# Performance work log

Hardware: AMD Instinct MI355X
Metric: run time of the kernel (lower is better)

Reference implementation:

```python
import jax, jax.numpy as jnp
import numpy as np

B, T, C, H = 8, 4096, 1024, 128

def setup_inputs() -> dict:
    key = jax.random.key(0)
    k1, k2, k3, k4 = jax.random.split(key, 4)
    x = jax.random.normal(k1, (B, T, C), dtype=jnp.float32)
    # torch Linear default init scale ~ 1/sqrt(fan_in); use scaled normal
    s = 1.0 / np.sqrt(C)
    Wq = jax.random.normal(k2, (C, H), dtype=jnp.float32) * s
    Wk = jax.random.normal(k3, (C, H), dtype=jnp.float32) * s
    Wv = jax.random.normal(k4, (C, H), dtype=jnp.float32) * s
    return {"x": x, "Wq": Wq, "Wk": Wk, "Wv": Wv}

def reference(x, Wq, Wk, Wv):
    # q,k,v: [B,T,H]
    q = jnp.einsum('btc,ch->bth', x, Wq)
    k = jnp.einsum('btc,ch->bth', x, Wk)
    v = jnp.einsum('btc,ch->bth', x, Wv)
    scale = k.shape[-1] ** -0.5
    wei = jnp.einsum('bqh,bkh->bqk', q, k) * scale  # [B,T,T]
    causal = jnp.tril(jnp.ones((T, T), dtype=bool))
    wei = jnp.where(causal, wei, -jnp.inf)
    wei = jax.nn.softmax(wei, axis=-1)
    # dropout p=0.0 (eval): identity
    out = jnp.einsum('bqk,bkh->bqh', wei, v)  # [B,T,H]
    return out
```

## Files before the change

### kernel.cpp

```cpp
#include <hip/hip_runtime.h>

#define B_ 8
#define T_ 4096
#define C_ 1024
#define H_ 128

using bf16x8 = __attribute__((ext_vector_type(8))) __bf16;
using bf16x4 = __attribute__((ext_vector_type(4))) __bf16;
using f32x4  = __attribute__((ext_vector_type(4))) float;

__device__ __forceinline__ unsigned short f2bf(float f) {
    union { float f; unsigned u; } v; v.f = f;
    unsigned u = v.u;
    u += 0x7FFF + ((u >> 16) & 1);
    return (unsigned short)(u >> 16);
}
__device__ __forceinline__ ushort4 pack4(const f32x4 v) {
    ushort4 p; p.x = f2bf(v[0]); p.y = f2bf(v[1]); p.z = f2bf(v[2]); p.w = f2bf(v[3]);
    return p;
}
__device__ __forceinline__ ushort4 pack4f(const float4 v) {
    ushort4 p; p.x = f2bf(v.x); p.y = f2bf(v.y); p.z = f2bf(v.z); p.w = f2bf(v.w);
    return p;
}

__global__ __launch_bounds__(256) void wt_kernel(const float* __restrict__ Wq,
                                                 const float* __restrict__ Wk,
                                                 const float* __restrict__ Wv,
                                                 unsigned short* __restrict__ wt) {
    int idx = blockIdx.x * 256 + threadIdx.x;
    int w = idx / (C_ * H_);
    int r = idx - w * (C_ * H_);
    int c = r >> 7;
    int h = r & (H_ - 1);
    const float* W = (w == 0) ? Wq : (w == 1) ? Wk : Wv;
    wt[((size_t)w * H_ + h) * C_ + c] = f2bf(W[r]);
}

#define PLDA 40
__global__ __launch_bounds__(256, 4) void proj_kernel(
        const float* __restrict__ x, const unsigned short* __restrict__ wt,
        unsigned short* __restrict__ q, unsigned short* __restrict__ k,
        unsigned short* __restrict__ vt) {
    __shared__ unsigned short Xs[2][64 * PLDA];
    __shared__ unsigned short Ws[2][128 * PLDA];
    const int widx = blockIdx.x;
    const int mt   = blockIdx.y;
    const int tid  = threadIdx.x;
    const int wave = tid >> 6, lane = tid & 63, quad = lane >> 4, l16 = lane & 15;
    const int r0 = (wave >> 1) * 32;
    const int c0 = (wave & 1) * 64;
    const size_t m0 = (size_t)mt * 64;
    const unsigned short* wtw = wt + (size_t)widx * H_ * C_;

    const int xrow = tid >> 3, xcol = (tid & 7) * 4;
    const int wrow = tid >> 2, wcol = (tid & 3) * 8;

    float4 xr0, xr1; uint4 wr0, wr1;
    auto LOADXW = [&](int k0) {
        const float* xp = x + m0 * C_ + k0;
        xr0 = *(const float4*)(xp + (size_t)(xrow)      * C_ + xcol);
        xr1 = *(const float4*)(xp + (size_t)(xrow + 32) * C_ + xcol);
        const unsigned short* wp = wtw + k0;
        wr0 = *(const uint4*)(wp + (size_t)(wrow)      * C_ + wcol);
        wr1 = *(const uint4*)(wp + (size_t)(wrow + 64) * C_ + wcol);
    };
    auto STOREXW = [&](int ibb) {
        *(ushort4*)&Xs[ibb][(xrow)      * PLDA + xcol] = pack4f(xr0);
        *(ushort4*)&Xs[ibb][(xrow + 32) * PLDA + xcol] = pack4f(xr1);
        *(uint4*)&Ws[ibb][(wrow)      * PLDA + wcol] = wr0;
        *(uint4*)&Ws[ibb][(wrow + 64) * PLDA + wcol] = wr1;
    };

    f32x4 acc[2][4];
    #pragma unroll
    for (int mi = 0; mi < 2; mi++)
        #pragma unroll
        for (int ni = 0; ni < 4; ni++)
            acc[mi][ni] = (f32x4){0.f, 0.f, 0.f, 0.f};

    LOADXW(0);
    STOREXW(0);
    int ib = 0;
    for (int k0 = 0; k0 < C_; k0 += 32, ib ^= 1) {
        __syncthreads();
        if (k0 + 32 < C_) LOADXW(k0 + 32);
        bf16x8 af[2], bfr[4];
        #pragma unroll
        for (int mi = 0; mi < 2; mi++)
            af[mi] = *(const bf16x8*)&Xs[ib][(r0 + mi * 16 + l16) * PLDA + quad * 8];
        #pragma unroll
        for (int ni = 0; ni < 4; ni++)
            bfr[ni] = *(const bf16x8*)&Ws[ib][(c0 + ni * 16 + l16) * PLDA + quad * 8];
        if (widx < 2) {
            #pragma unroll
            for (int mi = 0; mi < 2; mi++)
                #pragma unroll
                for (int ni = 0; ni < 4; ni++)
                    acc[mi][ni] = __builtin_amdgcn_mfma_f32_16x16x32_bf16(
                                      bfr[ni], af[mi], acc[mi][ni], 0, 0, 0);
        } else {
            #pragma unroll
            for (int mi = 0; mi < 2; mi++)
                #pragma unroll
                for (int ni = 0; ni < 4; ni++)
                    acc[mi][ni] = __builtin_amdgcn_mfma_f32_16x16x32_bf16(
                                      af[mi], bfr[ni], acc[mi][ni], 0, 0, 0);
        }
        if (k0 + 32 < C_) STOREXW(ib ^ 1);
    }

    if (widx < 2) {
        const float QS = (widx == 0) ? (1.4426950408889634f * 0.08838834764831845f) : 1.0f;
        unsigned short* dst = (widx == 0) ? q : k;
        #pragma unroll
        for (int mi = 0; mi < 2; mi++)
            #pragma unroll
            for (int ni = 0; ni < 4; ni++) {
                size_t xrow2 = m0 + r0 + mi * 16 + l16;
                int h0 = c0 + ni * 16 + quad * 4;
                f32x4 a = acc[mi][ni];
                a[0] *= QS; a[1] *= QS; a[2] *= QS; a[3] *= QS;
                *(ushort4*)&dst[xrow2 * H_ + h0] = pack4(a);
            }
    } else {
        #pragma unroll
        for (int mi = 0; mi < 2; mi++)
            #pragma unroll
            for (int ni = 0; ni < 4; ni++) {
                size_t m = m0 + r0 + mi * 16 + quad * 4;
                int bb = (int)(m >> 12);
                int t  = (int)(m & (T_ - 1));
                int h  = c0 + ni * 16 + l16;
                *(ushort4*)&vt[((size_t)bb * H_ + h) * T_ + t] = pack4(acc[mi][ni]);
            }
    }
}

#define FLDQ 136
#define FLDV 72
#define FLDP 72
__global__ __launch_bounds__(256, 2) void flash_kernel(
        const unsigned short* __restrict__ q,
        const unsigned short* __restrict__ kmat,
        const unsigned short* __restrict__ vt,
        float* __restrict__ out) {
    __shared__ unsigned short Ks[2][64 * FLDQ];
    __shared__ unsigned short Vs[2][H_ * FLDV];
    __shared__ unsigned short Ps[64 * FLDP];

    const int b  = blockIdx.y;
    const int xx = blockIdx.x;
    const int qt = (b < 4) ? xx : (63 - xx);
    const int tid = threadIdx.x;
    const int wave = tid >> 6, lane = tid & 63, quad = lane >> 4, l16 = lane & 15;
    const int mrow = wave * 16;

    const int krow = tid >> 4, kcol = (tid & 15) * 8;
    const int vrow = tid >> 3, vcol = (tid & 7) * 8;

    uint4 kr0, kr1, kr2, kr3, vr0, vr1, vr2, vr3;
    auto LOADKV = [&](int jj) {
        const unsigned short* kp = kmat + ((size_t)b * T_ + (size_t)jj * 64) * H_;
        const unsigned short* vp = vt + (size_t)b * H_ * T_ + (size_t)jj * 64;
        kr0 = *(const uint4*)(kp + (size_t)(krow)      * H_ + kcol);
        kr1 = *(const uint4*)(kp + (size_t)(krow + 16) * H_ + kcol);
        kr2 = *(const uint4*)(kp + (size_t)(krow + 32) * H_ + kcol);
        kr3 = *(const uint4*)(kp + (size_t)(krow + 48) * H_ + kcol);
        vr0 = *(const uint4*)(vp + (size_t)(vrow)      * T_ + vcol);
        vr1 = *(const uint4*)(vp + (size_t)(vrow + 32) * T_ + vcol);
        vr2 = *(const uint4*)(vp + (size_t)(vrow + 64) * T_ + vcol);
        vr3 = *(const uint4*)(vp + (size_t)(vrow + 96) * T_ + vcol);
    };
    auto STOREKV = [&](int ibb) {
        *(uint4*)&Ks[ibb][(krow)      * FLDQ + kcol] = kr0;
        *(uint4*)&Ks[ibb][(krow + 16) * FLDQ + kcol] = kr1;
        *(uint4*)&Ks[ibb][(krow + 32) * FLDQ + kcol] = kr2;
        *(uint4*)&Ks[ibb][(krow + 48) * FLDQ + kcol] = kr3;
        *(uint4*)&Vs[ibb][(vrow)      * FLDV + vcol] = vr0;
        *(uint4*)&Vs[ibb][(vrow + 32) * FLDV + vcol] = vr1;
        *(uint4*)&Vs[ibb][(vrow + 64) * FLDV + vcol] = vr2;
        *(uint4*)&Vs[ibb][(vrow + 96) * FLDV + vcol] = vr3;
    };

    const unsigned short* qp = q + ((size_t)b * T_ + (size_t)qt * 64) * H_;
    *(uint4*)&Ks[0][(krow)      * FLDQ + kcol] = *(const uint4*)(qp + (size_t)(krow)      * H_ + kcol);
    *(uint4*)&Ks[0][(krow + 16) * FLDQ + kcol] = *(const uint4*)(qp + (size_t)(krow + 16) * H_ + kcol);
    *(uint4*)&Ks[0][(krow + 32) * FLDQ + kcol] = *(const uint4*)(qp + (size_t)(krow + 32) * H_ + kcol);
    *(uint4*)&Ks[0][(krow + 48) * FLDQ + kcol] = *(const uint4*)(qp + (size_t)(krow + 48) * H_ + kcol);
    LOADKV(0);
    __syncthreads();
    bf16x8 aq[4];
    #pragma unroll
    for (int kk = 0; kk < 4; kk++)
        aq[kk] = *(const bf16x8*)&Ks[0][(mrow + l16) * FLDQ + kk * 32 + quad * 8];
    __syncthreads();
    STOREKV(0);

    bf16x8 a1;
    #pragma unroll
    for (int z = 0; z < 8; z++) a1[z] = (__bf16)1.0f;

    f32x4 o[9];
    #pragma unroll
    for (int nt = 0; nt < 9; nt++) o[nt] = (f32x4){0.f, 0.f, 0.f, 0.f};

    const int tq = qt * 64 + mrow + l16;

    int ib = 0;
    for (int j = 0; j <= qt; j++, ib ^= 1) {
        __syncthreads();
        if (j < qt) LOADKV(j + 1);

        f32x4 s[4];
        #pragma unroll
        for (int mi = 0; mi < 4; mi++) s[mi] = (f32x4){0.f, 0.f, 0.f, 0.f};
        __builtin_amdgcn_s_setprio(1);
        #pragma unroll
        for (int kk = 0; kk < 4; kk++) {
            #pragma unroll
            for (int mi = 0; mi < 4; mi++) {
                bf16x8 ak = *(const bf16x8*)&Ks[ib][(mi * 16 + l16) * FLDQ + kk * 32 + quad * 8];
                s[mi] = __builtin_amdgcn_mfma_f32_16x16x32_bf16(ak, aq[kk], s[mi], 0, 0, 0);
            }
        }
        __builtin_amdgcn_s_setprio(0);
        if (j == qt) {
            #pragma unroll
            for (int mi = 0; mi < 4; mi++)
                #pragma unroll
                for (int r = 0; r < 4; r++) {
                    int tk = j * 64 + mi * 16 + quad * 4 + r;
                    if (tk > tq) s[mi][r] = -__builtin_inff();
                }
        }

        #pragma unroll
        for (int mi = 0; mi < 4; mi++) {
            bf16x4 pb;
            #pragma unroll
            for (int r = 0; r < 4; r++)
                pb[r] = (__bf16)exp2f(s[mi][r] - 16.0f);
            *(bf16x4*)&Ps[(mrow + l16) * FLDP + mi * 16 + quad * 4] = pb;
        }

        asm volatile("s_waitcnt lgkmcnt(0)" ::: "memory");

        __builtin_amdgcn_s_setprio(1);
        #pragma unroll
        for (int ks = 0; ks < 2; ks++) {
            bf16x8 bp = *(const bf16x8*)&Ps[(mrow + l16) * FLDP + ks * 32 + quad * 8];
            #pragma unroll
            for (int nt = 0; nt < 8; nt++) {
                bf16x8 av = *(const bf16x8*)&Vs[ib][(nt * 16 + l16) * FLDV + ks * 32 + quad * 8];
                o[nt] = __builtin_amdgcn_mfma_f32_16x16x32_bf16(av, bp, o[nt], 0, 0, 0);
            }
            o[8] = __builtin_amdgcn_mfma_f32_16x16x32_bf16(a1, bp, o[8], 0, 0, 0);
        }
        __builtin_amdgcn_s_setprio(0);

        if (j < qt) STOREKV(ib ^ 1);
    }

    float inv = 1.0f / o[8][0];
    size_t row = (size_t)b * T_ + (size_t)qt * 64 + mrow + l16;
    #pragma unroll
    for (int nt = 0; nt < 8; nt++) {
        float4 ov;
        ov.x = o[nt][0] * inv; ov.y = o[nt][1] * inv;
        ov.z = o[nt][2] * inv; ov.w = o[nt][3] * inv;
        *(float4*)&out[row * H_ + nt * 16 + quad * 4] = ov;
    }
}

extern "C" void kernel_launch(void* const* d_in, const int* in_sizes, int n_in,
                              void* d_out, int out_size, void* d_ws, size_t ws_size,
                              hipStream_t stream) {
    const float* x  = (const float*)d_in[0];
    const float* Wq = (const float*)d_in[1];
    const float* Wk = (const float*)d_in[2];
    const float* Wv = (const float*)d_in[3];
    float* out = (float*)d_out;

    unsigned short* ws  = (unsigned short*)d_ws;
    const size_t nqkv   = (size_t)B_ * T_ * H_;
    unsigned short* qb  = ws;
    unsigned short* kb  = qb + nqkv;
    unsigned short* vtb = kb + nqkv;
    unsigned short* wt  = vtb + nqkv;

    wt_kernel<<<dim3((3 * C_ * H_) / 256), dim3(256), 0, stream>>>(Wq, Wk, Wv, wt);
    proj_kernel<<<dim3(3, (B_ * T_) / 64), dim3(256), 0, stream>>>(x, wt, qb, kb, vtb);
    flash_kernel<<<dim3(T_ / 64, B_), dim3(256), 0, stream>>>(qb, kb, vtb, out);
}
```

Baseline: 340.3 us.

## Enlarge projection tile to 128 rows, remap blocks for XCD locality, drop setprio

The projection GEMM now computes 128-row tiles per block instead of 64, doubling reuse of each weight tile per x load and halving the block count. Block ids are remapped so the three weight projections for the same rows are interleaved across XCDs, and the weight transpose kernel now writes coalesced instead of reading coalesced. The flash kernel's s_setprio hints around the MFMA sections are removed. Larger tiles raise register and LDS use, so occupancy is lowered to 3 blocks per CU.

```diff
diff --git a/kernel.cpp b/kernel.cpp
--- a/kernel.cpp
+++ b/kernel.cpp
@@ -29,52 +29,55 @@
                                                  const float* __restrict__ Wv,
                                                  unsigned short* __restrict__ wt) {
     int idx = blockIdx.x * 256 + threadIdx.x;
-    int w = idx / (C_ * H_);
-    int r = idx - w * (C_ * H_);
-    int c = r >> 7;
-    int h = r & (H_ - 1);
+    int c = idx & (C_ - 1);
+    int h = (idx >> 10) & (H_ - 1);
+    int w = idx >> 17;
     const float* W = (w == 0) ? Wq : (w == 1) ? Wk : Wv;
-    wt[((size_t)w * H_ + h) * C_ + c] = f2bf(W[r]);
+    wt[idx] = f2bf(W[c * H_ + h]);
 }
 
 #define PLDA 40
-__global__ __launch_bounds__(256, 4) void proj_kernel(
+__global__ __launch_bounds__(256, 3) void proj_kernel(
         const float* __restrict__ x, const unsigned short* __restrict__ wt,
         unsigned short* __restrict__ q, unsigned short* __restrict__ k,
         unsigned short* __restrict__ vt) {
-    __shared__ unsigned short Xs[2][64 * PLDA];
+    __shared__ unsigned short Xs[2][128 * PLDA];
     __shared__ unsigned short Ws[2][128 * PLDA];
-    const int widx = blockIdx.x;
-    const int mt   = blockIdx.y;
+    const int bid  = blockIdx.x;
+    const int work = (bid & 7) * 96 + (bid >> 3);
+    const int mt   = work / 3;
+    const int widx = work - mt * 3;
     const int tid  = threadIdx.x;
     const int wave = tid >> 6, lane = tid & 63, quad = lane >> 4, l16 = lane & 15;
-    const int r0 = (wave >> 1) * 32;
+    const int r0 = (wave >> 1) * 64;
     const int c0 = (wave & 1) * 64;
-    const size_t m0 = (size_t)mt * 64;
+    const size_t m0 = (size_t)mt * 128;
     const unsigned short* wtw = wt + (size_t)widx * H_ * C_;
 
     const int xrow = tid >> 3, xcol = (tid & 7) * 4;
     const int wrow = tid >> 2, wcol = (tid & 3) * 8;
 
-    float4 xr0, xr1; uint4 wr0, wr1;
+    float4 xr[4]; uint4 wr0, wr1;
     auto LOADXW = [&](int k0) {
         const float* xp = x + m0 * C_ + k0;
-        xr0 = *(const float4*)(xp + (size_t)(xrow)      * C_ + xcol);
-        xr1 = *(const float4*)(xp + (size_t)(xrow + 32) * C_ + xcol);
+        #pragma unroll
+        for (int c = 0; c < 4; c++)
+            xr[c] = *(const float4*)(xp + (size_t)(xrow + 32 * c) * C_ + xcol);
         const unsigned short* wp = wtw + k0;
         wr0 = *(const uint4*)(wp + (size_t)(wrow)      * C_ + wcol);
         wr1 = *(const uint4*)(wp + (size_t)(wrow + 64) * C_ + wcol);
     };
     auto STOREXW = [&](int ibb) {
-        *(ushort4*)&Xs[ibb][(xrow)      * PLDA + xcol] = pack4f(xr0);
-        *(ushort4*)&Xs[ibb][(xrow + 32) * PLDA + xcol] = pack4f(xr1);
+        #pragma unroll
+        for (int c = 0; c < 4; c++)
+            *(ushort4*)&Xs[ibb][(xrow + 32 * c) * PLDA + xcol] = pack4f(xr[c]);
         *(uint4*)&Ws[ibb][(wrow)      * PLDA + wcol] = wr0;
         *(uint4*)&Ws[ibb][(wrow + 64) * PLDA + wcol] = wr1;
     };
 
-    f32x4 acc[2][4];
-    #pragma unroll
-    for (int mi = 0; mi < 2; mi++)
+    f32x4 acc[4][4];
+    #pragma unroll
+    for (int mi = 0; mi < 4; mi++)
         #pragma unroll
         for (int ni = 0; ni < 4; ni++)
             acc[mi][ni] = (f32x4){0.f, 0.f, 0.f, 0.f};
@@ -85,23 +88,23 @@
     for (int k0 = 0; k0 < C_; k0 += 32, ib ^= 1) {
         __syncthreads();
         if (k0 + 32 < C_) LOADXW(k0 + 32);
-        bf16x8 af[2], bfr[4];
-        #pragma unroll
-        for (int mi = 0; mi < 2; mi++)
+        bf16x8 af[4], bfr[4];
+        #pragma unroll
+        for (int mi = 0; mi < 4; mi++)
             af[mi] = *(const bf16x8*)&Xs[ib][(r0 + mi * 16 + l16) * PLDA + quad * 8];
         #pragma unroll
         for (int ni = 0; ni < 4; ni++)
             bfr[ni] = *(const bf16x8*)&Ws[ib][(c0 + ni * 16 + l16) * PLDA + quad * 8];
         if (widx < 2) {
             #pragma unroll
-            for (int mi = 0; mi < 2; mi++)
+            for (int mi = 0; mi < 4; mi++)
                 #pragma unroll
                 for (int ni = 0; ni < 4; ni++)
                     acc[mi][ni] = __builtin_amdgcn_mfma_f32_16x16x32_bf16(
                                       bfr[ni], af[mi], acc[mi][ni], 0, 0, 0);
         } else {
             #pragma unroll
-            for (int mi = 0; mi < 2; mi++)
+            for (int mi = 0; mi < 4; mi++)
                 #pragma unroll
                 for (int ni = 0; ni < 4; ni++)
                     acc[mi][ni] = __builtin_amdgcn_mfma_f32_16x16x32_bf16(
@@ -114,7 +117,7 @@
         const float QS = (widx == 0) ? (1.4426950408889634f * 0.08838834764831845f) : 1.0f;
         unsigned short* dst = (widx == 0) ? q : k;
         #pragma unroll
-        for (int mi = 0; mi < 2; mi++)
+        for (int mi = 0; mi < 4; mi++)
             #pragma unroll
             for (int ni = 0; ni < 4; ni++) {
                 size_t xrow2 = m0 + r0 + mi * 16 + l16;
@@ -125,7 +128,7 @@
             }
     } else {
         #pragma unroll
-        for (int mi = 0; mi < 2; mi++)
+        for (int mi = 0; mi < 4; mi++)
             #pragma unroll
             for (int ni = 0; ni < 4; ni++) {
                 size_t m = m0 + r0 + mi * 16 + quad * 4;
@@ -215,7 +218,6 @@
         f32x4 s[4];
         #pragma unroll
         for (int mi = 0; mi < 4; mi++) s[mi] = (f32x4){0.f, 0.f, 0.f, 0.f};
-        __builtin_amdgcn_s_setprio(1);
         #pragma unroll
         for (int kk = 0; kk < 4; kk++) {
             #pragma unroll
@@ -224,7 +226,6 @@
                 s[mi] = __builtin_amdgcn_mfma_f32_16x16x32_bf16(ak, aq[kk], s[mi], 0, 0, 0);
             }
         }
-        __builtin_amdgcn_s_setprio(0);
         if (j == qt) {
             #pragma unroll
             for (int mi = 0; mi < 4; mi++)
@@ -246,7 +247,6 @@
 
         asm volatile("s_waitcnt lgkmcnt(0)" ::: "memory");
 
-        __builtin_amdgcn_s_setprio(1);
         #pragma unroll
         for (int ks = 0; ks < 2; ks++) {
             bf16x8 bp = *(const bf16x8*)&Ps[(mrow + l16) * FLDP + ks * 32 + quad * 8];
@@ -257,7 +257,6 @@
             }
             o[8] = __builtin_amdgcn_mfma_f32_16x16x32_bf16(a1, bp, o[8], 0, 0, 0);
         }
-        __builtin_amdgcn_s_setprio(0);
 
         if (j < qt) STOREKV(ib ^ 1);
     }
@@ -290,6 +289,6 @@
     unsigned short* wt  = vtb + nqkv;
 
     wt_kernel<<<dim3((3 * C_ * H_) / 256), dim3(256), 0, stream>>>(Wq, Wk, Wv, wt);
-    proj_kernel<<<dim3(3, (B_ * T_) / 64), dim3(256), 0, stream>>>(x, wt, qb, kb, vtb);
+    proj_kernel<<<dim3(3 * (B_ * T_) / 128), dim3(256), 0, stream>>>(x, wt, qb, kb, vtb);
     flash_kernel<<<dim3(T_ / 64, B_), dim3(256), 0, stream>>>(qb, kb, vtb, out);
 }
```

After: 670.0 us. 1.97x slower.
